# Optimization experiments

Measured on AMD Instinct MI355X. Metric: run time of the kernel, lower is better.

The kernel has to match this reference:

```python
import jax, jax.numpy as jnp
import numpy as np

N = 100000
E = 600000
IN_DIM = 256
H0 = 128
H1 = 64
EPS = 1e-5


def setup_inputs() -> dict:
    key = jax.random.key(0)
    ks = jax.random.split(key, 12)
    x = jax.random.normal(ks[0], (N, IN_DIM), dtype=jnp.float32)
    edge_index = jax.random.randint(ks[1], (2, E), 0, N, dtype=jnp.int64)
    edge_weight = jax.random.uniform(ks[2], (E,), dtype=jnp.float32)
    def lin(k, fan_in, fan_out):
        bound = 1.0 / np.sqrt(fan_in)
        k1, k2 = jax.random.split(k)
        W = jax.random.uniform(k1, (fan_in, fan_out), minval=-bound, maxval=bound, dtype=jnp.float32)
        b = jax.random.uniform(k2, (fan_out,), minval=-bound, maxval=bound, dtype=jnp.float32)
        return W, b
    W0, b0 = lin(ks[3], IN_DIM, H0)
    W1, b1 = lin(ks[4], H0, H0)
    W2, b2 = lin(ks[5], H0, H0)
    pW, pb = lin(ks[6], H0, H1)
    return {
        'x': x, 'edge_index': edge_index, 'edge_weight': edge_weight,
        'bn_gamma': jnp.ones((IN_DIM,), jnp.float32), 'bn_beta': jnp.zeros((IN_DIM,), jnp.float32),
        'W0': W0, 'b0': b0, 'W1': W1, 'b1': b1, 'W2': W2, 'b2': b2,
        'pbn_gamma': jnp.ones((H0,), jnp.float32), 'pbn_beta': jnp.zeros((H0,), jnp.float32),
        'pW': pW, 'pb': pb,
    }


def batchnorm(x, gamma, beta):
    # BatchNorm1d training-mode forward: per-feature batch statistics over nodes
    mean = jnp.mean(x, axis=0)
    var = jnp.mean(jnp.square(x - mean), axis=0)  # biased var, as torch BN forward
    return (x - mean) * jax.lax.rsqrt(var + EPS) * gamma + beta


def gcn_conv(x, src, dst, norm, W, b):
    # PyG GCNConv (add_self_loops=False): transform then normalized aggregation
    h = x @ W                                   # [N, out]
    msg = norm[:, None] * h[src]                # gather + scale, [E, out]
    out = jax.ops.segment_sum(msg, dst, num_segments=N)  # scatter-add
    return out + b


def reference(x, edge_index, edge_weight, bn_gamma, bn_beta, W0, b0, W1, b1, W2, b2, pbn_gamma, pbn_beta, pW, pb):
    src, dst = edge_index[0], edge_index[1]
    # gcn_norm without self loops: D^-1/2 A D^-1/2
    deg = jax.ops.segment_sum(edge_weight, dst, num_segments=N)
    dis = jnp.where(deg > 0, jax.lax.rsqrt(jnp.maximum(deg, EPS)), 0.0)
    norm = dis[src] * edge_weight * dis[dst]    # [E]

    h = batchnorm(x, bn_gamma, bn_beta)
    h = jax.nn.relu(gcn_conv(h, src, dst, norm, W0, b0))
    h = jax.nn.relu(gcn_conv(h, src, dst, norm, W1, b1))
    h = jax.nn.relu(gcn_conv(h, src, dst, norm, W2, b2))
    # project head: BN -> Linear -> ReLU
    h = batchnorm(h, pbn_gamma, pbn_beta)
    h = jax.nn.relu(h @ pW + pb)
    return h
```

## Files before the change

kernel.cpp:

```cpp
#include <hip/hip_runtime.h>


constexpr int NN     = 100000;
constexpr int NEDGE  = 600000;
constexpr int INDIM  = 256;
constexpr int HD     = 128;
constexpr int OUTD   = 64;
#define EPSV 1e-5f

typedef __bf16 bf16x8 __attribute__((ext_vector_type(8)));
typedef float  f32x4  __attribute__((ext_vector_type(4)));

__device__ __forceinline__ float bf2f(unsigned short u) {
    unsigned int v = ((unsigned int)u) << 16;
    return __builtin_bit_cast(float, v);
}
__device__ __forceinline__ unsigned short f2bf(float f) {
    __bf16 h = (__bf16)f;
    return __builtin_bit_cast(unsigned short, h);
}
__device__ __forceinline__ void atomAdd(float* p, float v) {
    unsafeAtomicAdd(p, v);
}

__global__ __launch_bounds__(256) void deghist_k(const int* __restrict__ dst,
                                                 const float* __restrict__ ew,
                                                 float* __restrict__ deg,
                                                 int* __restrict__ cnt, int e) {
    int i = blockIdx.x * blockDim.x + threadIdx.x;
    if (i < e) {
        int d = dst[i];
        atomAdd(&deg[d], ew[i]);
        atomicAdd(&cnt[d], 1);
    }
}

__global__ __launch_bounds__(256) void scan1_k(const int* __restrict__ cnt,
                                               int* __restrict__ rowptr,
                                               int* __restrict__ bsum, int n) {
    __shared__ int s[256];
    int i = blockIdx.x * 256 + threadIdx.x;
    s[threadIdx.x] = (i < n) ? cnt[i] : 0;
    __syncthreads();
    for (int d = 1; d < 256; d <<= 1) {
        int t = (threadIdx.x >= d) ? s[threadIdx.x - d] : 0;
        __syncthreads();
        s[threadIdx.x] += t;
        __syncthreads();
    }
    if (i < n) rowptr[i + 1] = s[threadIdx.x];
    if (threadIdx.x == 255) bsum[blockIdx.x] = s[255];
}

__global__ __launch_bounds__(512) void scan2_k(int* __restrict__ bsum, int nb) {
    __shared__ int s[512];
    s[threadIdx.x] = (threadIdx.x < (unsigned)nb) ? bsum[threadIdx.x] : 0;
    __syncthreads();
    for (int d = 1; d < 512; d <<= 1) {
        int t = (threadIdx.x >= d) ? s[threadIdx.x - d] : 0;
        __syncthreads();
        s[threadIdx.x] += t;
        __syncthreads();
    }
    if (threadIdx.x < (unsigned)nb) bsum[threadIdx.x] = s[threadIdx.x];
}

__global__ __launch_bounds__(256) void scan3_k(int* __restrict__ rowptr,
                                               const int* __restrict__ bsum,
                                               int* __restrict__ cursor, int n) {
    int i = blockIdx.x * 256 + threadIdx.x;
    if (i == 0) { rowptr[0] = 0; cursor[0] = 0; }
    if (i < n) {
        int v = rowptr[i + 1];
        if (blockIdx.x > 0) v += bsum[blockIdx.x - 1];
        rowptr[i + 1] = v;
        if (i + 1 < n) cursor[i + 1] = v;
    }
}

__global__ __launch_bounds__(256) void scatter_k(const int* __restrict__ src,
                                                 const int* __restrict__ dst,
                                                 const float* __restrict__ ew,
                                                 const float* __restrict__ deg,
                                                 int* __restrict__ cursor,
                                                 uint2* __restrict__ edata, int e) {
    int i = blockIdx.x * blockDim.x + threadIdx.x;
    if (i < e) {
        int s = src[i], d = dst[i];
        float ds = deg[s], dd = deg[d];
        float is = ds > 0.f ? rsqrtf(fmaxf(ds, EPSV)) : 0.f;
        float id = dd > 0.f ? rsqrtf(fmaxf(dd, EPSV)) : 0.f;
        float nm = is * ew[i] * id;
        int p = atomicAdd(&cursor[d], 1);
        edata[p] = make_uint2((unsigned)s, __builtin_bit_cast(unsigned, nm));
    }
}

__global__ __launch_bounds__(256) void bn_stats_x_k(const float* __restrict__ in,
                                                    float* __restrict__ sums,
                                                    unsigned short* __restrict__ xb,
                                                    int n) {
    const int tid = threadIdx.x;
    const int cg  = tid & 63;
    const int rs  = tid >> 6;
    float s0 = 0.f, s1 = 0.f, s2 = 0.f, s3 = 0.f;
    float q0 = 0.f, q1 = 0.f, q2 = 0.f, q3 = 0.f;
    for (int r0 = blockIdx.x * 16; r0 < n; r0 += gridDim.x * 16) {
        float4 v[4];
#pragma unroll
        for (int j = 0; j < 4; j++)
            v[j] = *(const float4*)&in[(size_t)(r0 + rs + j * 4) * INDIM + cg * 4];
#pragma unroll
        for (int j = 0; j < 4; j++) {
            s0 += v[j].x; s1 += v[j].y; s2 += v[j].z; s3 += v[j].w;
            q0 += v[j].x * v[j].x; q1 += v[j].y * v[j].y;
            q2 += v[j].z * v[j].z; q3 += v[j].w * v[j].w;
            unsigned int w0 = (unsigned int)f2bf(v[j].x) | ((unsigned int)f2bf(v[j].y) << 16);
            unsigned int w1 = (unsigned int)f2bf(v[j].z) | ((unsigned int)f2bf(v[j].w) << 16);
            *(uint2*)&xb[(size_t)(r0 + rs + j * 4) * INDIM + cg * 4] = make_uint2(w0, w1);
        }
    }
    __shared__ float red[256 * 8];
    red[tid * 8 + 0] = s0; red[tid * 8 + 1] = s1;
    red[tid * 8 + 2] = s2; red[tid * 8 + 3] = s3;
    red[tid * 8 + 4] = q0; red[tid * 8 + 5] = q1;
    red[tid * 8 + 6] = q2; red[tid * 8 + 7] = q3;
    __syncthreads();
    int cgr = tid >> 2, j = tid & 3;
    float a = 0.f, b = 0.f;
#pragma unroll
    for (int r2 = 0; r2 < 4; r2++) {
        a += red[(r2 * 64 + cgr) * 8 + j];
        b += red[(r2 * 64 + cgr) * 8 + 4 + j];
    }
    atomAdd(&sums[tid], a);
    atomAdd(&sums[INDIM + tid], b);
}

__global__ __launch_bounds__(256) void bn_stats16_k(const unsigned short* __restrict__ in,
                                                    float* __restrict__ sums, int n) {
    const int tid = threadIdx.x;
    const int cg  = tid & 15;
    const int rs  = tid >> 4;
    float s[8], q[8];
#pragma unroll
    for (int j = 0; j < 8; j++) { s[j] = 0.f; q[j] = 0.f; }
    for (int r = blockIdx.x * 16 + rs; r < n; r += gridDim.x * 16) {
        uint4 u = *(const uint4*)&in[(size_t)r * HD + cg * 8];
        float v[8];
        v[0] = bf2f((unsigned short)(u.x & 0xffff)); v[1] = bf2f((unsigned short)(u.x >> 16));
        v[2] = bf2f((unsigned short)(u.y & 0xffff)); v[3] = bf2f((unsigned short)(u.y >> 16));
        v[4] = bf2f((unsigned short)(u.z & 0xffff)); v[5] = bf2f((unsigned short)(u.z >> 16));
        v[6] = bf2f((unsigned short)(u.w & 0xffff)); v[7] = bf2f((unsigned short)(u.w >> 16));
#pragma unroll
        for (int j = 0; j < 8; j++) { s[j] += v[j]; q[j] += v[j] * v[j]; }
    }
    __shared__ float red[256 * 16];
#pragma unroll
    for (int j = 0; j < 8; j++) {
        red[tid * 16 + j]     = s[j];
        red[tid * 16 + 8 + j] = q[j];
    }
    __syncthreads();
    if (tid < HD) {
        int cgr = tid >> 3, j = tid & 7;
        float a = 0.f, b = 0.f;
#pragma unroll
        for (int r2 = 0; r2 < 16; r2++) {
            a += red[(r2 * 16 + cgr) * 16 + j];
            b += red[(r2 * 16 + cgr) * 16 + 8 + j];
        }
        atomAdd(&sums[tid], a);
        atomAdd(&sums[HD + tid], b);
    }
}

__global__ __launch_bounds__(256) void wprep1_k(const float* __restrict__ stats,
                                                const float* __restrict__ gamma,
                                                const float* __restrict__ beta,
                                                const float* __restrict__ W0,
                                                const float* __restrict__ W1,
                                                const float* __restrict__ W2,
                                                unsigned short* __restrict__ W0t,
                                                unsigned short* __restrict__ W1t,
                                                unsigned short* __restrict__ W2t,
                                                float* __restrict__ d0, float invN) {
    __shared__ float sA[INDIM], sC[INDIM];
    int f = threadIdx.x;
    {
        float mean = stats[f] * invN;
        float var  = stats[INDIM + f] * invN - mean * mean;
        float a    = gamma[f] * rsqrtf(var + EPSV);
        sA[f] = a;
        sC[f] = beta[f] - mean * a;
    }
    __syncthreads();
    int b = blockIdx.x, tid = threadIdx.x;
    if (b < 128) {
        int i = b * 256 + tid, k = i >> 7, j = i & 127;
        W0t[(size_t)j * INDIM + k] = f2bf(W0[i] * sA[k]);
    } else if (b < 192) {
        int i = (b - 128) * 256 + tid, k = i >> 7, j = i & 127;
        W1t[(size_t)j * HD + k] = f2bf(W1[i]);
    } else if (b < 256) {
        int i = (b - 192) * 256 + tid, k = i >> 7, j = i & 127;
        W2t[(size_t)j * HD + k] = f2bf(W2[i]);
    } else {
        if (tid < HD) {
            float s = 0.f;
            for (int ff = 0; ff < INDIM; ff++) s += sC[ff] * W0[ff * HD + tid];
            d0[tid] = s;
        }
    }
}

__global__ __launch_bounds__(256) void wprep2_k(const float* __restrict__ stats2,
                                                const float* __restrict__ gamma,
                                                const float* __restrict__ beta,
                                                const float* __restrict__ pW,
                                                const float* __restrict__ pb,
                                                unsigned short* __restrict__ pWt,
                                                float* __restrict__ dfin, float invN) {
    __shared__ float sA[HD], sC[HD];
    int f = threadIdx.x;
    if (f < HD) {
        float mean = stats2[f] * invN;
        float var  = stats2[HD + f] * invN - mean * mean;
        float a    = gamma[f] * rsqrtf(var + EPSV);
        sA[f] = a;
        sC[f] = beta[f] - mean * a;
    }
    __syncthreads();
    int b = blockIdx.x, tid = threadIdx.x;
    if (b < 32) {
        int i = b * 256 + tid, k = i >> 6, j = i & 63;
        pWt[(size_t)j * HD + k] = f2bf(pW[i] * sA[k]);
    } else {
        if (tid < OUTD) {
            float s = pb[tid];
            for (int ff = 0; ff < HD; ff++) s += sC[ff] * pW[ff * OUTD + tid];
            dfin[tid] = s;
        }
    }
}

template <int K, int M, bool RELU_OUT, bool OUT_BF16>
__global__ __launch_bounds__(256) void mgemm_k(const unsigned short* __restrict__ A,
                                               const unsigned short* __restrict__ Bt,
                                               const float* __restrict__ outBias,
                                               void* __restrict__ Craw, int n) {
    constexpr int BK  = 64;
    constexpr int LDA = BK + 8;
    __shared__ unsigned short As[128 * LDA];
    __shared__ unsigned short Bs[M * LDA];

    const int tid  = threadIdx.x;
    const int wave = tid >> 6, lane = tid & 63;
    const int quad = lane >> 4, mrow = lane & 15;
    const int row0 = blockIdx.x * 128;

    constexpr int RT = (M == 128) ? 4 : 2;
    constexpr int CT = 4;
    const int rowbase = (M == 128) ? ((wave >> 1) * 64) : (wave * 32);
    const int colbase = (M == 128) ? ((wave & 1) * 64) : 0;

    f32x4 acc[RT][CT];
#pragma unroll
    for (int i = 0; i < RT; i++)
#pragma unroll
        for (int j = 0; j < CT; j++) acc[i][j] = (f32x4){0.f, 0.f, 0.f, 0.f};

    for (int k0 = 0; k0 < K; k0 += BK) {
#pragma unroll
        for (int p = 0; p < 4; p++) {
            int c   = p * 256 + tid;
            int r   = c >> 3;
            int c8  = (c & 7) * 8;
            int grow = row0 + r;
            uint4 u = make_uint4(0, 0, 0, 0);
            if (grow < n) u = *(const uint4*)&A[(size_t)grow * K + k0 + c8];
            *(uint4*)&As[r * LDA + c8] = u;
        }
#pragma unroll
        for (int p = 0; p < M / 32; p++) {
            int c  = p * 256 + tid;
            int r  = c >> 3;
            int c8 = (c & 7) * 8;
            *(uint4*)&Bs[r * LDA + c8] = *(const uint4*)&Bt[(size_t)r * K + k0 + c8];
        }
        __syncthreads();

#pragma unroll
        for (int ks = 0; ks < BK; ks += 32) {
            bf16x8 af[RT], bfr[CT];
#pragma unroll
            for (int i = 0; i < RT; i++)
                af[i] = *(const bf16x8*)&As[(rowbase + i * 16 + mrow) * LDA + ks + quad * 8];
#pragma unroll
            for (int j = 0; j < CT; j++)
                bfr[j] = *(const bf16x8*)&Bs[(colbase + j * 16 + mrow) * LDA + ks + quad * 8];
#pragma unroll
            for (int i = 0; i < RT; i++)
#pragma unroll
                for (int j = 0; j < CT; j++)
                    acc[i][j] = __builtin_amdgcn_mfma_f32_16x16x32_bf16(
                        af[i], bfr[j], acc[i][j], 0, 0, 0);
        }
        __syncthreads();
    }

#pragma unroll
    for (int i = 0; i < RT; i++) {
#pragma unroll
        for (int r = 0; r < 4; r++) {
            int row = row0 + rowbase + i * 16 + quad * 4 + r;
            if (row < n) {
#pragma unroll
                for (int j = 0; j < CT; j++) {
                    int col = colbase + j * 16 + mrow;
                    float v = acc[i][j][r];
                    if (outBias) v += outBias[col];
                    if (RELU_OUT) v = fmaxf(v, 0.f);
                    if (OUT_BF16)
                        ((unsigned short*)Craw)[(size_t)row * M + col] = f2bf(v);
                    else
                        ((float*)Craw)[(size_t)row * M + col] = v;
                }
            }
        }
    }
}

__global__ __launch_bounds__(256) void agg_csr16_k(const unsigned short* __restrict__ t,
                                                   const int* __restrict__ rowptr,
                                                   const uint2* __restrict__ edata,
                                                   const float* __restrict__ bias,
                                                   unsigned short* __restrict__ agg,
                                                   int n) {
    const int tid  = threadIdx.x;
    const int g    = tid >> 4;
    const int gl   = tid & 15;
    const int node = blockIdx.x * 16 + g;
    if (node >= n) return;
    const int beg = rowptr[node], end = rowptr[node + 1];
    float acc[8];
#pragma unroll
    for (int j = 0; j < 8; j++) acc[j] = 0.f;
    const unsigned short* tg = t + gl * 8;
    for (int i = beg; i < end; i += 4) {
        uint4 v[4]; float w[4];
#pragma unroll
        for (int k = 0; k < 4; k++) {
            int  idx = i + k;
            bool ok  = idx < end;
            uint2 ed = edata[ok ? idx : beg];
            w[k] = ok ? __builtin_bit_cast(float, ed.y) : 0.f;
            v[k] = *(const uint4*)&tg[(size_t)ed.x * HD];
        }
#pragma unroll
        for (int k = 0; k < 4; k++) {
            acc[0] += w[k] * bf2f((unsigned short)(v[k].x & 0xffff));
            acc[1] += w[k] * bf2f((unsigned short)(v[k].x >> 16));
            acc[2] += w[k] * bf2f((unsigned short)(v[k].y & 0xffff));
            acc[3] += w[k] * bf2f((unsigned short)(v[k].y >> 16));
            acc[4] += w[k] * bf2f((unsigned short)(v[k].z & 0xffff));
            acc[5] += w[k] * bf2f((unsigned short)(v[k].z >> 16));
            acc[6] += w[k] * bf2f((unsigned short)(v[k].w & 0xffff));
            acc[7] += w[k] * bf2f((unsigned short)(v[k].w >> 16));
        }
    }
    float4 b0 = *(const float4*)&bias[gl * 8];
    float4 b1 = *(const float4*)&bias[gl * 8 + 4];
    float r0 = fmaxf(acc[0] + b0.x, 0.f), r1 = fmaxf(acc[1] + b0.y, 0.f);
    float r2 = fmaxf(acc[2] + b0.z, 0.f), r3 = fmaxf(acc[3] + b0.w, 0.f);
    float r4 = fmaxf(acc[4] + b1.x, 0.f), r5 = fmaxf(acc[5] + b1.y, 0.f);
    float r6 = fmaxf(acc[6] + b1.z, 0.f), r7 = fmaxf(acc[7] + b1.w, 0.f);
    uint4 o;
    o.x = (unsigned int)f2bf(r0) | ((unsigned int)f2bf(r1) << 16);
    o.y = (unsigned int)f2bf(r2) | ((unsigned int)f2bf(r3) << 16);
    o.z = (unsigned int)f2bf(r4) | ((unsigned int)f2bf(r5) << 16);
    o.w = (unsigned int)f2bf(r6) | ((unsigned int)f2bf(r7) << 16);
    *(uint4*)&agg[(size_t)node * HD + gl * 8] = o;
}

extern "C" void kernel_launch(void* const* d_in, const int* in_sizes, int n_in,
                              void* d_out, int out_size, void* d_ws, size_t ws_size,
                              hipStream_t stream) {
    const float* x        = (const float*)d_in[0];
    const int*   ei       = (const int*)d_in[1];
    const float* ew       = (const float*)d_in[2];
    const float* bn_gamma = (const float*)d_in[3];
    const float* bn_beta  = (const float*)d_in[4];
    const float* W0       = (const float*)d_in[5];
    const float* b0       = (const float*)d_in[6];
    const float* W1       = (const float*)d_in[7];
    const float* b1       = (const float*)d_in[8];
    const float* W2       = (const float*)d_in[9];
    const float* b2       = (const float*)d_in[10];
    const float* pgamma   = (const float*)d_in[11];
    const float* pbeta    = (const float*)d_in[12];
    const float* pW       = (const float*)d_in[13];
    const float* pb       = (const float*)d_in[14];
    float* out = (float*)d_out;

    const int* srcp = ei;
    const int* dstp = ei + NEDGE;

    char*  base = (char*)d_ws;
    size_t off  = 0;
    auto carve = [&](size_t bytes) -> void* {
        void* p = (void*)(base + off);
        off = (off + bytes + 255) & ~(size_t)255;
        return p;
    };
    float*          deg    = (float*)carve(NN * 4);
    int*            cnt    = (int*)carve(NN * 4);
    float*          stats  = (float*)carve(2 * INDIM * 4);
    float*          stats2 = (float*)carve(2 * HD * 4);
    int*            rowptr = (int*)carve((NN + 1) * 4);
    int*            cursor = (int*)carve(NN * 4);
    int*            bsum   = (int*)carve(512 * 4);
    uint2*          edata  = (uint2*)carve((size_t)NEDGE * 8);
    float*          d0     = (float*)carve(HD * 4);
    float*          dfin   = (float*)carve(OUTD * 4);
    unsigned short* W0t    = (unsigned short*)carve((size_t)INDIM * HD * 2);
    unsigned short* W1t    = (unsigned short*)carve((size_t)HD * HD * 2);
    unsigned short* W2t    = (unsigned short*)carve((size_t)HD * HD * 2);
    unsigned short* pWt    = (unsigned short*)carve((size_t)HD * OUTD * 2);
    unsigned short* xb     = (unsigned short*)carve((size_t)NN * INDIM * 2);
    unsigned short* tbuf   = (unsigned short*)carve((size_t)NN * HD * 2);
    unsigned short* aggb   = (unsigned short*)carve((size_t)NN * HD * 2);
    (void)ws_size;

    const int eBlocks  = (NEDGE + 255) / 256;
    const int nBlocks  = (NN + 255) / 256;
    const int gemmGrid = (NN + 127) / 128;
    const int aggGrid  = (NN + 15) / 16;

    hipMemsetAsync(deg, 0, (size_t)((char*)cnt - (char*)deg) + NN * 4, stream);
    hipMemsetAsync(stats, 0, (size_t)((char*)stats2 - (char*)stats) + 2 * HD * 4, stream);

    deghist_k<<<eBlocks, 256, 0, stream>>>(dstp, ew, deg, cnt, NEDGE);
    scan1_k<<<nBlocks, 256, 0, stream>>>(cnt, rowptr, bsum, NN);
    scan2_k<<<1, 512, 0, stream>>>(bsum, nBlocks);
    scan3_k<<<nBlocks, 256, 0, stream>>>(rowptr, bsum, cursor, NN);
    scatter_k<<<eBlocks, 256, 0, stream>>>(srcp, dstp, ew, deg, cursor, edata, NEDGE);

    bn_stats_x_k<<<1024, 256, 0, stream>>>(x, stats, xb, NN);
    wprep1_k<<<257, 256, 0, stream>>>(stats, bn_gamma, bn_beta, W0, W1, W2,
                                      W0t, W1t, W2t, d0, 1.f / NN);

    mgemm_k<INDIM, HD, false, true><<<gemmGrid, 256, 0, stream>>>(
        xb, W0t, d0, tbuf, NN);
    agg_csr16_k<<<aggGrid, 256, 0, stream>>>(tbuf, rowptr, edata, b0, aggb, NN);

    mgemm_k<HD, HD, false, true><<<gemmGrid, 256, 0, stream>>>(
        aggb, W1t, nullptr, tbuf, NN);
    agg_csr16_k<<<aggGrid, 256, 0, stream>>>(tbuf, rowptr, edata, b1, aggb, NN);

    mgemm_k<HD, HD, false, true><<<gemmGrid, 256, 0, stream>>>(
        aggb, W2t, nullptr, tbuf, NN);
    agg_csr16_k<<<aggGrid, 256, 0, stream>>>(tbuf, rowptr, edata, b2, aggb, NN);

    bn_stats16_k<<<512, 256, 0, stream>>>(aggb, stats2, NN);
    wprep2_k<<<33, 256, 0, stream>>>(stats2, pgamma, pbeta, pW, pb, pWt, dfin,
                                     1.f / NN);
    mgemm_k<HD, OUTD, true, false><<<gemmGrid, 256, 0, stream>>>(
        aggb, pWt, dfin, out, NN);

    (void)n_in; (void)in_sizes; (void)out_size;
}
```

Before: 484.2 us.

## Fuse GCN aggregation with next-layer GEMM and merge independent setup kernels

Merges independent preprocessing kernels into combined launches split by block index: degree histogram with BN stats, scan with weight prep, and edge scatter with the first GEMM. It also fuses each CSR aggregation with the following layer's MFMA GEMM through shared memory, and fuses the last aggregation with the BN statistics pass. The goal is to cut kernel launch count and avoid writing and re-reading the intermediate aggregated activations in global memory. In exchange, the fused aggregate+GEMM kernel runs only one 128-row block per tile with heavy shared memory use, which may lower occupancy for the latency-bound gather phase.

New measurement: 474.2 us. 1.02x faster.

```diff
diff --git a/kernel.cpp b/kernel.cpp
--- a/kernel.cpp
+++ b/kernel.cpp
@@ -1,11 +1,17 @@
 #include <hip/hip_runtime.h>
 
 
-constexpr int NN     = 100000;
-constexpr int NEDGE  = 600000;
-constexpr int INDIM  = 256;
-constexpr int HD     = 128;
-constexpr int OUTD   = 64;
+constexpr int NN    = 100000;
+constexpr int NEDGE = 600000;
+constexpr int INDIM = 256;
+constexpr int HD    = 128;
+constexpr int OUTD  = 64;
+constexpr int EB    = (NEDGE + 255) / 256;
+constexpr int SB    = 1024;
+constexpr int NB    = (NN + 255) / 256;
+constexpr int WB    = 257;
+constexpr int GG    = (NN + 127) / 128;
+constexpr int A2B   = 1024;
 #define EPSV 1e-5f
 
 typedef __bf16 bf16x8 __attribute__((ext_vector_type(8)));
@@ -23,93 +29,245 @@
     unsafeAtomicAdd(p, v);
 }
 
-__global__ __launch_bounds__(256) void deghist_k(const int* __restrict__ dst,
-                                                 const float* __restrict__ ew,
-                                                 float* __restrict__ deg,
-                                                 int* __restrict__ cnt, int e) {
-    int i = blockIdx.x * blockDim.x + threadIdx.x;
-    if (i < e) {
-        int d = dst[i];
-        atomAdd(&deg[d], ew[i]);
-        atomicAdd(&cnt[d], 1);
-    }
-}
-
-__global__ __launch_bounds__(256) void scan1_k(const int* __restrict__ cnt,
-                                               int* __restrict__ rowptr,
-                                               int* __restrict__ bsum, int n) {
-    __shared__ int s[256];
-    int i = blockIdx.x * 256 + threadIdx.x;
-    s[threadIdx.x] = (i < n) ? cnt[i] : 0;
-    __syncthreads();
-    for (int d = 1; d < 256; d <<= 1) {
-        int t = (threadIdx.x >= d) ? s[threadIdx.x - d] : 0;
+template <int K, int M, bool RELU_OUT, bool OUT_BF16>
+__device__ __forceinline__ void mgemm_body(int bid, int tid, char* smem,
+                                           const unsigned short* __restrict__ A,
+                                           const unsigned short* __restrict__ Bt,
+                                           const float* __restrict__ outBias,
+                                           void* __restrict__ Craw, int n) {
+    constexpr int BK  = 64;
+    constexpr int LDA = BK + 8;
+    unsigned short* As = (unsigned short*)smem;
+    unsigned short* Bs = As + 128 * LDA;
+
+    const int wave = tid >> 6, lane = tid & 63;
+    const int quad = lane >> 4, mrow = lane & 15;
+    const int row0 = bid * 128;
+
+    constexpr int RT = (M == 128) ? 4 : 2;
+    constexpr int CT = 4;
+    const int rowbase = (M == 128) ? ((wave >> 1) * 64) : (wave * 32);
+    const int colbase = (M == 128) ? ((wave & 1) * 64) : 0;
+
+    f32x4 acc[RT][CT];
+#pragma unroll
+    for (int i = 0; i < RT; i++)
+#pragma unroll
+        for (int j = 0; j < CT; j++) acc[i][j] = (f32x4){0.f, 0.f, 0.f, 0.f};
+
+    for (int k0 = 0; k0 < K; k0 += BK) {
+        if (k0) __syncthreads();
+#pragma unroll
+        for (int p = 0; p < 4; p++) {
+            int c   = p * 256 + tid;
+            int r   = c >> 3;
+            int c8  = (c & 7) * 8;
+            int grow = row0 + r;
+            uint4 u = make_uint4(0, 0, 0, 0);
+            if (grow < n) u = *(const uint4*)&A[(size_t)grow * K + k0 + c8];
+            *(uint4*)&As[r * LDA + c8] = u;
+        }
+#pragma unroll
+        for (int p = 0; p < M / 32; p++) {
+            int c  = p * 256 + tid;
+            int r  = c >> 3;
+            int c8 = (c & 7) * 8;
+            *(uint4*)&Bs[r * LDA + c8] = *(const uint4*)&Bt[(size_t)r * K + k0 + c8];
+        }
         __syncthreads();
-        s[threadIdx.x] += t;
+
+#pragma unroll
+        for (int ks = 0; ks < BK; ks += 32) {
+            bf16x8 af[RT], bfr[CT];
+#pragma unroll
+            for (int i = 0; i < RT; i++)
+                af[i] = *(const bf16x8*)&As[(rowbase + i * 16 + mrow) * LDA + ks + quad * 8];
+#pragma unroll
+            for (int j = 0; j < CT; j++)
+                bfr[j] = *(const bf16x8*)&Bs[(colbase + j * 16 + mrow) * LDA + ks + quad * 8];
+#pragma unroll
+            for (int i = 0; i < RT; i++)
+#pragma unroll
+                for (int j = 0; j < CT; j++)
+                    acc[i][j] = __builtin_amdgcn_mfma_f32_16x16x32_bf16(
+                        af[i], bfr[j], acc[i][j], 0, 0, 0);
+        }
+    }
+
+#pragma unroll
+    for (int i = 0; i < RT; i++) {
+#pragma unroll
+        for (int r = 0; r < 4; r++) {
+            int row = row0 + rowbase + i * 16 + quad * 4 + r;
+            if (row < n) {
+#pragma unroll
+                for (int j = 0; j < CT; j++) {
+                    int col = colbase + j * 16 + mrow;
+                    float v = acc[i][j][r];
+                    if (outBias) v += outBias[col];
+                    if (RELU_OUT) v = fmaxf(v, 0.f);
+                    if (OUT_BF16)
+                        ((unsigned short*)Craw)[(size_t)row * M + col] = f2bf(v);
+                    else
+                        ((float*)Craw)[(size_t)row * M + col] = v;
+                }
+            }
+        }
+    }
+}
+
+__device__ __forceinline__ void gather8(const unsigned short* __restrict__ tg,
+                                        const uint2* __restrict__ edata,
+                                        int i, int beg, int end, float* acc) {
+    uint4 v[8]; float w[8];
+#pragma unroll
+    for (int k = 0; k < 8; k++) {
+        int  idx = i + k;
+        bool ok  = idx < end;
+        uint2 ed = edata[ok ? idx : beg];
+        w[k] = ok ? __builtin_bit_cast(float, ed.y) : 0.f;
+        v[k] = *(const uint4*)&tg[(size_t)ed.x * HD];
+    }
+#pragma unroll
+    for (int k = 0; k < 8; k++) {
+        acc[0] += w[k] * bf2f((unsigned short)(v[k].x & 0xffff));
+        acc[1] += w[k] * bf2f((unsigned short)(v[k].x >> 16));
+        acc[2] += w[k] * bf2f((unsigned short)(v[k].y & 0xffff));
+        acc[3] += w[k] * bf2f((unsigned short)(v[k].y >> 16));
+        acc[4] += w[k] * bf2f((unsigned short)(v[k].z & 0xffff));
+        acc[5] += w[k] * bf2f((unsigned short)(v[k].z >> 16));
+        acc[6] += w[k] * bf2f((unsigned short)(v[k].w & 0xffff));
+        acc[7] += w[k] * bf2f((unsigned short)(v[k].w >> 16));
+    }
+}
+
+__global__ __launch_bounds__(256) void fagg_gemm_k(const unsigned short* __restrict__ t,
+                                                   const int* __restrict__ rowptr,
+                                                   const uint2* __restrict__ edata,
+                                                   const float* __restrict__ bias,
+                                                   const unsigned short* __restrict__ Bt,
+                                                   unsigned short* __restrict__ Cout,
+                                                   int n) {
+    constexpr int LDAa = HD + 8;
+    constexpr int LDAb = 64 + 8;
+    __shared__ unsigned short As[128 * LDAa];
+    __shared__ unsigned short Bs[HD * LDAb];
+
+    const int tid  = threadIdx.x;
+    const int row0 = blockIdx.x * 128;
+
+    {
+        const int g  = tid >> 4;
+        const int gl = tid & 15;
+        const unsigned short* tg = t + gl * 8;
+        float4 bb0 = *(const float4*)&bias[gl * 8];
+        float4 bb1 = *(const float4*)&bias[gl * 8 + 4];
+        for (int rr = 0; rr < 8; rr++) {
+            int node = row0 + g * 8 + rr;
+            float acc[8];
+#pragma unroll
+            for (int j = 0; j < 8; j++) acc[j] = 0.f;
+            if (node < n) {
+                int beg = rowptr[node], end = rowptr[node + 1];
+                for (int i = beg; i < end; i += 8)
+                    gather8(tg, edata, i, beg, end, acc);
+            }
+            float r0 = fmaxf(acc[0] + bb0.x, 0.f), r1 = fmaxf(acc[1] + bb0.y, 0.f);
+            float r2 = fmaxf(acc[2] + bb0.z, 0.f), r3 = fmaxf(acc[3] + bb0.w, 0.f);
+            float r4 = fmaxf(acc[4] + bb1.x, 0.f), r5 = fmaxf(acc[5] + bb1.y, 0.f);
+            float r6 = fmaxf(acc[6] + bb1.z, 0.f), r7 = fmaxf(acc[7] + bb1.w, 0.f);
+            uint4 o;
+            o.x = (unsigned int)f2bf(r0) | ((unsigned int)f2bf(r1) << 16);
+            o.y = (unsigned int)f2bf(r2) | ((unsigned int)f2bf(r3) << 16);
+            o.z = (unsigned int)f2bf(r4) | ((unsigned int)f2bf(r5) << 16);
+            o.w = (unsigned int)f2bf(r6) | ((unsigned int)f2bf(r7) << 16);
+            *(uint4*)&As[(g * 8 + rr) * LDAa + gl * 8] = o;
+        }
+    }
+
+    const int wave = tid >> 6, lane = tid & 63;
+    const int quad = lane >> 4, mrow = lane & 15;
+    const int rowbase = (wave >> 1) * 64;
+    const int colbase = (wave & 1) * 64;
+
+    f32x4 acc[4][4];
+#pragma unroll
+    for (int i = 0; i < 4; i++)
+#pragma unroll
+        for (int j = 0; j < 4; j++) acc[i][j] = (f32x4){0.f, 0.f, 0.f, 0.f};
+
+    for (int k0 = 0; k0 < HD; k0 += 64) {
+        if (k0) __syncthreads();
+#pragma unroll
+        for (int p = 0; p < 4; p++) {
+            int c  = p * 256 + tid;
+            int r  = c >> 3;
+            int c8 = (c & 7) * 8;
+            *(uint4*)&Bs[r * LDAb + c8] = *(const uint4*)&Bt[(size_t)r * HD + k0 + c8];
+        }
         __syncthreads();
-    }
-    if (i < n) rowptr[i + 1] = s[threadIdx.x];
-    if (threadIdx.x == 255) bsum[blockIdx.x] = s[255];
-}
-
-__global__ __launch_bounds__(512) void scan2_k(int* __restrict__ bsum, int nb) {
-    __shared__ int s[512];
-    s[threadIdx.x] = (threadIdx.x < (unsigned)nb) ? bsum[threadIdx.x] : 0;
-    __syncthreads();
-    for (int d = 1; d < 512; d <<= 1) {
-        int t = (threadIdx.x >= d) ? s[threadIdx.x - d] : 0;
-        __syncthreads();
-        s[threadIdx.x] += t;
-        __syncthreads();
-    }
-    if (threadIdx.x < (unsigned)nb) bsum[threadIdx.x] = s[threadIdx.x];
-}
-
-__global__ __launch_bounds__(256) void scan3_k(int* __restrict__ rowptr,
-                                               const int* __restrict__ bsum,
-                                               int* __restrict__ cursor, int n) {
-    int i = blockIdx.x * 256 + threadIdx.x;
-    if (i == 0) { rowptr[0] = 0; cursor[0] = 0; }
-    if (i < n) {
-        int v = rowptr[i + 1];
-        if (blockIdx.x > 0) v += bsum[blockIdx.x - 1];
-        rowptr[i + 1] = v;
-        if (i + 1 < n) cursor[i + 1] = v;
-    }
-}
-
-__global__ __launch_bounds__(256) void scatter_k(const int* __restrict__ src,
-                                                 const int* __restrict__ dst,
-                                                 const float* __restrict__ ew,
-                                                 const float* __restrict__ deg,
-                                                 int* __restrict__ cursor,
-                                                 uint2* __restrict__ edata, int e) {
-    int i = blockIdx.x * blockDim.x + threadIdx.x;
-    if (i < e) {
-        int s = src[i], d = dst[i];
-        float ds = deg[s], dd = deg[d];
-        float is = ds > 0.f ? rsqrtf(fmaxf(ds, EPSV)) : 0.f;
-        float id = dd > 0.f ? rsqrtf(fmaxf(dd, EPSV)) : 0.f;
-        float nm = is * ew[i] * id;
-        int p = atomicAdd(&cursor[d], 1);
-        edata[p] = make_uint2((unsigned)s, __builtin_bit_cast(unsigned, nm));
-    }
-}
-
-__global__ __launch_bounds__(256) void bn_stats_x_k(const float* __restrict__ in,
-                                                    float* __restrict__ sums,
-                                                    unsigned short* __restrict__ xb,
-                                                    int n) {
+#pragma unroll
+        for (int ks = 0; ks < 64; ks += 32) {
+            bf16x8 af[4], bfr[4];
+#pragma unroll
+            for (int i = 0; i < 4; i++)
+                af[i] = *(const bf16x8*)&As[(rowbase + i * 16 + mrow) * LDAa + k0 + ks + quad * 8];
+#pragma unroll
+            for (int j = 0; j < 4; j++)
+                bfr[j] = *(const bf16x8*)&Bs[(colbase + j * 16 + mrow) * LDAb + ks + quad * 8];
+#pragma unroll
+            for (int i = 0; i < 4; i++)
+#pragma unroll
+                for (int j = 0; j < 4; j++)
+                    acc[i][j] = __builtin_amdgcn_mfma_f32_16x16x32_bf16(
+                        af[i], bfr[j], acc[i][j], 0, 0, 0);
+        }
+    }
+
+#pragma unroll
+    for (int i = 0; i < 4; i++) {
+#pragma unroll
+        for (int r = 0; r < 4; r++) {
+            int row = row0 + rowbase + i * 16 + quad * 4 + r;
+            if (row < n) {
+#pragma unroll
+                for (int j = 0; j < 4; j++) {
+                    int col = colbase + j * 16 + mrow;
+                    Cout[(size_t)row * HD + col] = f2bf(acc[i][j][r]);
+                }
+            }
+        }
+    }
+}
+
+__global__ __launch_bounds__(256) void front_k(const int* __restrict__ dst,
+                                               const float* __restrict__ ew,
+                                               float* __restrict__ deg,
+                                               int* __restrict__ cnt,
+                                               const float* __restrict__ x,
+                                               float* __restrict__ sums,
+                                               unsigned short* __restrict__ xb) {
+    __shared__ float red[256 * 8];
     const int tid = threadIdx.x;
+    if (blockIdx.x < EB) {
+        int i = blockIdx.x * 256 + tid;
+        if (i < NEDGE) {
+            int d = dst[i];
+            atomAdd(&deg[d], ew[i]);
+            atomicAdd(&cnt[d], 1);
+        }
+        return;
+    }
+    const int bid = blockIdx.x - EB;
     const int cg  = tid & 63;
     const int rs  = tid >> 6;
     float s0 = 0.f, s1 = 0.f, s2 = 0.f, s3 = 0.f;
     float q0 = 0.f, q1 = 0.f, q2 = 0.f, q3 = 0.f;
-    for (int r0 = blockIdx.x * 16; r0 < n; r0 += gridDim.x * 16) {
+    for (int r0 = bid * 16; r0 < NN; r0 += SB * 16) {
         float4 v[4];
 #pragma unroll
         for (int j = 0; j < 4; j++)
-            v[j] = *(const float4*)&in[(size_t)(r0 + rs + j * 4) * INDIM + cg * 4];
+            v[j] = *(const float4*)&x[(size_t)(r0 + rs + j * 4) * INDIM + cg * 4];
 #pragma unroll
         for (int j = 0; j < 4; j++) {
             s0 += v[j].x; s1 += v[j].y; s2 += v[j].z; s3 += v[j].w;
@@ -120,7 +278,6 @@
             *(uint2*)&xb[(size_t)(r0 + rs + j * 4) * INDIM + cg * 4] = make_uint2(w0, w1);
         }
     }
-    __shared__ float red[256 * 8];
     red[tid * 8 + 0] = s0; red[tid * 8 + 1] = s1;
     red[tid * 8 + 2] = s2; red[tid * 8 + 3] = s3;
     red[tid * 8 + 4] = q0; red[tid * 8 + 5] = q1;
@@ -137,65 +294,47 @@
     atomAdd(&sums[INDIM + tid], b);
 }
 
-__global__ __launch_bounds__(256) void bn_stats16_k(const unsigned short* __restrict__ in,
-                                                    float* __restrict__ sums, int n) {
+__global__ __launch_bounds__(256) void mid_k(const int* __restrict__ cnt,
+                                             int* __restrict__ rowptr,
+                                             int* __restrict__ bsum,
+                                             const float* __restrict__ stats,
+                                             const float* __restrict__ gamma,
+                                             const float* __restrict__ beta,
+                                             const float* __restrict__ W0,
+                                             const float* __restrict__ W1,
+                                             const float* __restrict__ W2,
+                                             unsigned short* __restrict__ W0t,
+                                             unsigned short* __restrict__ W1t,
+                                             unsigned short* __restrict__ W2t,
+                                             float* __restrict__ d0, float invN) {
+    __shared__ float sm[512];
     const int tid = threadIdx.x;
-    const int cg  = tid & 15;
-    const int rs  = tid >> 4;
-    float s[8], q[8];
-#pragma unroll
-    for (int j = 0; j < 8; j++) { s[j] = 0.f; q[j] = 0.f; }
-    for (int r = blockIdx.x * 16 + rs; r < n; r += gridDim.x * 16) {
-        uint4 u = *(const uint4*)&in[(size_t)r * HD + cg * 8];
-        float v[8];
-        v[0] = bf2f((unsigned short)(u.x & 0xffff)); v[1] = bf2f((unsigned short)(u.x >> 16));
-        v[2] = bf2f((unsigned short)(u.y & 0xffff)); v[3] = bf2f((unsigned short)(u.y >> 16));
-        v[4] = bf2f((unsigned short)(u.z & 0xffff)); v[5] = bf2f((unsigned short)(u.z >> 16));
-        v[6] = bf2f((unsigned short)(u.w & 0xffff)); v[7] = bf2f((unsigned short)(u.w >> 16));
-#pragma unroll
-        for (int j = 0; j < 8; j++) { s[j] += v[j]; q[j] += v[j] * v[j]; }
-    }
-    __shared__ float red[256 * 16];
-#pragma unroll
-    for (int j = 0; j < 8; j++) {
-        red[tid * 16 + j]     = s[j];
-        red[tid * 16 + 8 + j] = q[j];
+    if (blockIdx.x < NB) {
+        int* s = (int*)sm;
+        int i = blockIdx.x * 256 + tid;
+        s[tid] = (i < NN) ? cnt[i] : 0;
+        __syncthreads();
+        for (int d = 1; d < 256; d <<= 1) {
+            int t = (tid >= d) ? s[tid - d] : 0;
+            __syncthreads();
+            s[tid] += t;
+            __syncthreads();
+        }
+        if (i < NN) rowptr[i + 1] = s[tid];
+        if (tid == 255) bsum[blockIdx.x] = s[255];
+        return;
+    }
+    const int b = blockIdx.x - NB;
+    float* sA = sm;
+    float* sC = sm + 256;
+    {
+        float mean = stats[tid] * invN;
+        float var  = stats[INDIM + tid] * invN - mean * mean;
+        float a    = gamma[tid] * rsqrtf(var + EPSV);
+        sA[tid] = a;
+        sC[tid] = beta[tid] - mean * a;
     }
     __syncthreads();
-    if (tid < HD) {
-        int cgr = tid >> 3, j = tid & 7;
-        float a = 0.f, b = 0.f;
-#pragma unroll
-        for (int r2 = 0; r2 < 16; r2++) {
-            a += red[(r2 * 16 + cgr) * 16 + j];
-            b += red[(r2 * 16 + cgr) * 16 + 8 + j];
-        }
-        atomAdd(&sums[tid], a);
-        atomAdd(&sums[HD + tid], b);
-    }
-}
-
-__global__ __launch_bounds__(256) void wprep1_k(const float* __restrict__ stats,
-                                                const float* __restrict__ gamma,
-                                                const float* __restrict__ beta,
-                                                const float* __restrict__ W0,
-                                                const float* __restrict__ W1,
-                                                const float* __restrict__ W2,
-                                                unsigned short* __restrict__ W0t,
-                                                unsigned short* __restrict__ W1t,
-                                                unsigned short* __restrict__ W2t,
-                                                float* __restrict__ d0, float invN) {
-    __shared__ float sA[INDIM], sC[INDIM];
-    int f = threadIdx.x;
-    {
-        float mean = stats[f] * invN;
-        float var  = stats[INDIM + f] * invN - mean * mean;
-        float a    = gamma[f] * rsqrtf(var + EPSV);
-        sA[f] = a;
-        sC[f] = beta[f] - mean * a;
-    }
-    __syncthreads();
-    int b = blockIdx.x, tid = threadIdx.x;
     if (b < 128) {
         int i = b * 256 + tid, k = i >> 7, j = i & 127;
         W0t[(size_t)j * INDIM + k] = f2bf(W0[i] * sA[k]);
@@ -211,6 +350,121 @@
             for (int ff = 0; ff < INDIM; ff++) s += sC[ff] * W0[ff * HD + tid];
             d0[tid] = s;
         }
+    }
+}
+
+__global__ __launch_bounds__(512) void scan2_k(int* __restrict__ bsum, int nb) {
+    __shared__ int s[512];
+    s[threadIdx.x] = (threadIdx.x < (unsigned)nb) ? bsum[threadIdx.x] : 0;
+    __syncthreads();
+    for (int d = 1; d < 512; d <<= 1) {
+        int t = (threadIdx.x >= d) ? s[threadIdx.x - d] : 0;
+        __syncthreads();
+        s[threadIdx.x] += t;
+        __syncthreads();
+    }
+    if (threadIdx.x < (unsigned)nb) bsum[threadIdx.x] = s[threadIdx.x];
+}
+
+__global__ __launch_bounds__(256) void scan3_k(int* __restrict__ rowptr,
+                                               const int* __restrict__ bsum,
+                                               int* __restrict__ cursor, int n) {
+    int i = blockIdx.x * 256 + threadIdx.x;
+    if (i == 0) { rowptr[0] = 0; cursor[0] = 0; }
+    if (i < n) {
+        int v = rowptr[i + 1];
+        if (blockIdx.x > 0) v += bsum[blockIdx.x - 1];
+        rowptr[i + 1] = v;
+        if (i + 1 < n) cursor[i + 1] = v;
+    }
+}
+
+__global__ __launch_bounds__(256) void sg0_k(const int* __restrict__ src,
+                                             const int* __restrict__ dst,
+                                             const float* __restrict__ ew,
+                                             const float* __restrict__ deg,
+                                             int* __restrict__ cursor,
+                                             uint2* __restrict__ edata,
+                                             const unsigned short* __restrict__ xb,
+                                             const unsigned short* __restrict__ W0t,
+                                             const float* __restrict__ d0,
+                                             unsigned short* __restrict__ tbufA) {
+    __shared__ char smem[(128 * 72 + 128 * 72) * 2];
+    if (blockIdx.x < EB) {
+        int i = blockIdx.x * 256 + threadIdx.x;
+        if (i < NEDGE) {
+            int s = src[i], d = dst[i];
+            float ds = deg[s], dd = deg[d];
+            float is = ds > 0.f ? rsqrtf(fmaxf(ds, EPSV)) : 0.f;
+            float id = dd > 0.f ? rsqrtf(fmaxf(dd, EPSV)) : 0.f;
+            float nm = is * ew[i] * id;
+            int p = atomicAdd(&cursor[d], 1);
+            edata[p] = make_uint2((unsigned)s, __builtin_bit_cast(unsigned, nm));
+        }
+        return;
+    }
+    mgemm_body<INDIM, HD, false, true>(blockIdx.x - EB, threadIdx.x, smem,
+                                       xb, W0t, d0, tbufA, NN);
+}
+
+__global__ __launch_bounds__(256) void agg2_stats_k(const unsigned short* __restrict__ t,
+                                                    const int* __restrict__ rowptr,
+                                                    const uint2* __restrict__ edata,
+                                                    const float* __restrict__ bias,
+                                                    unsigned short* __restrict__ agg,
+                                                    float* __restrict__ sums, int n) {
+    const int tid = threadIdx.x, g = tid >> 4, gl = tid & 15;
+    const unsigned short* tg = t + gl * 8;
+    float4 bb0 = *(const float4*)&bias[gl * 8];
+    float4 bb1 = *(const float4*)&bias[gl * 8 + 4];
+    float ssum[8], ssq[8];
+#pragma unroll
+    for (int j = 0; j < 8; j++) { ssum[j] = 0.f; ssq[j] = 0.f; }
+
+    for (int node0 = blockIdx.x * 16; node0 < n; node0 += A2B * 16) {
+        int node = node0 + g;
+        float acc[8];
+#pragma unroll
+        for (int j = 0; j < 8; j++) acc[j] = 0.f;
+        if (node < n) {
+            int beg = rowptr[node], end = rowptr[node + 1];
+            for (int i = beg; i < end; i += 8)
+                gather8(tg, edata, i, beg, end, acc);
+        }
+        float r[8];
+        r[0] = fmaxf(acc[0] + bb0.x, 0.f); r[1] = fmaxf(acc[1] + bb0.y, 0.f);
+        r[2] = fmaxf(acc[2] + bb0.z, 0.f); r[3] = fmaxf(acc[3] + bb0.w, 0.f);
+        r[4] = fmaxf(acc[4] + bb1.x, 0.f); r[5] = fmaxf(acc[5] + bb1.y, 0.f);
+        r[6] = fmaxf(acc[6] + bb1.z, 0.f); r[7] = fmaxf(acc[7] + bb1.w, 0.f);
+        if (node < n) {
+            uint4 o;
+            o.x = (unsigned int)f2bf(r[0]) | ((unsigned int)f2bf(r[1]) << 16);
+            o.y = (unsigned int)f2bf(r[2]) | ((unsigned int)f2bf(r[3]) << 16);
+            o.z = (unsigned int)f2bf(r[4]) | ((unsigned int)f2bf(r[5]) << 16);
+            o.w = (unsigned int)f2bf(r[6]) | ((unsigned int)f2bf(r[7]) << 16);
+            *(uint4*)&agg[(size_t)node * HD + gl * 8] = o;
+#pragma unroll
+            for (int j = 0; j < 8; j++) { ssum[j] += r[j]; ssq[j] += r[j] * r[j]; }
+        }
+    }
+
+    __shared__ float red[256 * 16];
+#pragma unroll
+    for (int j = 0; j < 8; j++) {
+        red[tid * 16 + j]     = ssum[j];
+        red[tid * 16 + 8 + j] = ssq[j];
+    }
+    __syncthreads();
+    if (tid < HD) {
+        int glr = tid >> 3, j = tid & 7;
+        float a = 0.f, b = 0.f;
+#pragma unroll
+        for (int g2 = 0; g2 < 16; g2++) {
+            a += red[(g2 * 16 + glr) * 16 + j];
+            b += red[(g2 * 16 + glr) * 16 + 8 + j];
+        }
+        atomAdd(&sums[tid], a);
+        atomAdd(&sums[HD + tid], b);
     }
 }
 
@@ -244,143 +498,13 @@
     }
 }
 
-template <int K, int M, bool RELU_OUT, bool OUT_BF16>
-__global__ __launch_bounds__(256) void mgemm_k(const unsigned short* __restrict__ A,
+__global__ __launch_bounds__(256) void gemm3_k(const unsigned short* __restrict__ A,
                                                const unsigned short* __restrict__ Bt,
                                                const float* __restrict__ outBias,
-                                               void* __restrict__ Craw, int n) {
-    constexpr int BK  = 64;
-    constexpr int LDA = BK + 8;
-    __shared__ unsigned short As[128 * LDA];
-    __shared__ unsigned short Bs[M * LDA];
-
-    const int tid  = threadIdx.x;
-    const int wave = tid >> 6, lane = tid & 63;
-    const int quad = lane >> 4, mrow = lane & 15;
-    const int row0 = blockIdx.x * 128;
-
-    constexpr int RT = (M == 128) ? 4 : 2;
-    constexpr int CT = 4;
-    const int rowbase = (M == 128) ? ((wave >> 1) * 64) : (wave * 32);
-    const int colbase = (M == 128) ? ((wave & 1) * 64) : 0;
-
-    f32x4 acc[RT][CT];
-#pragma unroll
-    for (int i = 0; i < RT; i++)
-#pragma unroll
-        for (int j = 0; j < CT; j++) acc[i][j] = (f32x4){0.f, 0.f, 0.f, 0.f};
-
-    for (int k0 = 0; k0 < K; k0 += BK) {
-#pragma unroll
-        for (int p = 0; p < 4; p++) {
-            int c   = p * 256 + tid;
-            int r   = c >> 3;
-            int c8  = (c & 7) * 8;
-            int grow = row0 + r;
-            uint4 u = make_uint4(0, 0, 0, 0);
-            if (grow < n) u = *(const uint4*)&A[(size_t)grow * K + k0 + c8];
-            *(uint4*)&As[r * LDA + c8] = u;
-        }
-#pragma unroll
-        for (int p = 0; p < M / 32; p++) {
-            int c  = p * 256 + tid;
-            int r  = c >> 3;
-            int c8 = (c & 7) * 8;
-            *(uint4*)&Bs[r * LDA + c8] = *(const uint4*)&Bt[(size_t)r * K + k0 + c8];
-        }
-        __syncthreads();
-
-#pragma unroll
-        for (int ks = 0; ks < BK; ks += 32) {
-            bf16x8 af[RT], bfr[CT];
-#pragma unroll
-            for (int i = 0; i < RT; i++)
-                af[i] = *(const bf16x8*)&As[(rowbase + i * 16 + mrow) * LDA + ks + quad * 8];
-#pragma unroll
-            for (int j = 0; j < CT; j++)
-                bfr[j] = *(const bf16x8*)&Bs[(colbase + j * 16 + mrow) * LDA + ks + quad * 8];
-#pragma unroll
-            for (int i = 0; i < RT; i++)
-#pragma unroll
-                for (int j = 0; j < CT; j++)
-                    acc[i][j] = __builtin_amdgcn_mfma_f32_16x16x32_bf16(
-                        af[i], bfr[j], acc[i][j], 0, 0, 0);
-        }
-        __syncthreads();
-    }
-
-#pragma unroll
-    for (int i = 0; i < RT; i++) {
-#pragma unroll
-        for (int r = 0; r < 4; r++) {
-            int row = row0 + rowbase + i * 16 + quad * 4 + r;
-            if (row < n) {
-#pragma unroll
-                for (int j = 0; j < CT; j++) {
-                    int col = colbase + j * 16 + mrow;
-                    float v = acc[i][j][r];
-                    if (outBias) v += outBias[col];
-                    if (RELU_OUT) v = fmaxf(v, 0.f);
-                    if (OUT_BF16)
-                        ((unsigned short*)Craw)[(size_t)row * M + col] = f2bf(v);
-                    else
-                        ((float*)Craw)[(size_t)row * M + col] = v;
-                }
-            }
-        }
-    }
-}
-
-__global__ __launch_bounds__(256) void agg_csr16_k(const unsigned short* __restrict__ t,
-                                                   const int* __restrict__ rowptr,
-                                                   const uint2* __restrict__ edata,
-                                                   const float* __restrict__ bias,
-                                                   unsigned short* __restrict__ agg,
-                                                   int n) {
-    const int tid  = threadIdx.x;
-    const int g    = tid >> 4;
-    const int gl   = tid & 15;
-    const int node = blockIdx.x * 16 + g;
-    if (node >= n) return;
-    const int beg = rowptr[node], end = rowptr[node + 1];
-    float acc[8];
-#pragma unroll
-    for (int j = 0; j < 8; j++) acc[j] = 0.f;
-    const unsigned short* tg = t + gl * 8;
-    for (int i = beg; i < end; i += 4) {
-        uint4 v[4]; float w[4];
-#pragma unroll
-        for (int k = 0; k < 4; k++) {
-            int  idx = i + k;
-            bool ok  = idx < end;
-            uint2 ed = edata[ok ? idx : beg];
-            w[k] = ok ? __builtin_bit_cast(float, ed.y) : 0.f;
-            v[k] = *(const uint4*)&tg[(size_t)ed.x * HD];
-        }
-#pragma unroll
-        for (int k = 0; k < 4; k++) {
-            acc[0] += w[k] * bf2f((unsigned short)(v[k].x & 0xffff));
-            acc[1] += w[k] * bf2f((unsigned short)(v[k].x >> 16));
-            acc[2] += w[k] * bf2f((unsigned short)(v[k].y & 0xffff));
-            acc[3] += w[k] * bf2f((unsigned short)(v[k].y >> 16));
-            acc[4] += w[k] * bf2f((unsigned short)(v[k].z & 0xffff));
-            acc[5] += w[k] * bf2f((unsigned short)(v[k].z >> 16));
-            acc[6] += w[k] * bf2f((unsigned short)(v[k].w & 0xffff));
-            acc[7] += w[k] * bf2f((unsigned short)(v[k].w >> 16));
-        }
-    }
-    float4 b0 = *(const float4*)&bias[gl * 8];
-    float4 b1 = *(const float4*)&bias[gl * 8 + 4];
-    float r0 = fmaxf(acc[0] + b0.x, 0.f), r1 = fmaxf(acc[1] + b0.y, 0.f);
-    float r2 = fmaxf(acc[2] + b0.z, 0.f), r3 = fmaxf(acc[3] + b0.w, 0.f);
-    float r4 = fmaxf(acc[4] + b1.x, 0.f), r5 = fmaxf(acc[5] + b1.y, 0.f);
-    float r6 = fmaxf(acc[6] + b1.z, 0.f), r7 = fmaxf(acc[7] + b1.w, 0.f);
-    uint4 o;
-    o.x = (unsigned int)f2bf(r0) | ((unsigned int)f2bf(r1) << 16);
-    o.y = (unsigned int)f2bf(r2) | ((unsigned int)f2bf(r3) << 16);
-    o.z = (unsigned int)f2bf(r4) | ((unsigned int)f2bf(r5) << 16);
-    o.w = (unsigned int)f2bf(r6) | ((unsigned int)f2bf(r7) << 16);
-    *(uint4*)&agg[(size_t)node * HD + gl * 8] = o;
+                                               float* __restrict__ C, int n) {
+    __shared__ char smem[(128 * 72 + OUTD * 72) * 2];
+    mgemm_body<HD, OUTD, true, false>(blockIdx.x, threadIdx.x, smem,
+                                      A, Bt, outBias, C, n);
 }
 
 extern "C" void kernel_launch(void* const* d_in, const int* in_sizes, int n_in,
@@ -428,45 +552,31 @@
     unsigned short* W2t    = (unsigned short*)carve((size_t)HD * HD * 2);
     unsigned short* pWt    = (unsigned short*)carve((size_t)HD * OUTD * 2);
     unsigned short* xb     = (unsigned short*)carve((size_t)NN * INDIM * 2);
-    unsigned short* tbuf   = (unsigned short*)carve((size_t)NN * HD * 2);
+    unsigned short* tbufA  = (unsigned short*)carve((size_t)NN * HD * 2);
+    unsigned short* tbufB  = (unsigned short*)carve((size_t)NN * HD * 2);
     unsigned short* aggb   = (unsigned short*)carve((size_t)NN * HD * 2);
     (void)ws_size;
 
-    const int eBlocks  = (NEDGE + 255) / 256;
-    const int nBlocks  = (NN + 255) / 256;
-    const int gemmGrid = (NN + 127) / 128;
-    const int aggGrid  = (NN + 15) / 16;
-
-    hipMemsetAsync(deg, 0, (size_t)((char*)cnt - (char*)deg) + NN * 4, stream);
-    hipMemsetAsync(stats, 0, (size_t)((char*)stats2 - (char*)stats) + 2 * HD * 4, stream);
-
-    deghist_k<<<eBlocks, 256, 0, stream>>>(dstp, ew, deg, cnt, NEDGE);
-    scan1_k<<<nBlocks, 256, 0, stream>>>(cnt, rowptr, bsum, NN);
-    scan2_k<<<1, 512, 0, stream>>>(bsum, nBlocks);
-    scan3_k<<<nBlocks, 256, 0, stream>>>(rowptr, bsum, cursor, NN);
-    scatter_k<<<eBlocks, 256, 0, stream>>>(srcp, dstp, ew, deg, cursor, edata, NEDGE);
-
-    bn_stats_x_k<<<1024, 256, 0, stream>>>(x, stats, xb, NN);
-    wprep1_k<<<257, 256, 0, stream>>>(stats, bn_gamma, bn_beta, W0, W1, W2,
-                                      W0t, W1t, W2t, d0, 1.f / NN);
-
-    mgemm_k<INDIM, HD, false, true><<<gemmGrid, 256, 0, stream>>>(
-        xb, W0t, d0, tbuf, NN);
-    agg_csr16_k<<<aggGrid, 256, 0, stream>>>(tbuf, rowptr, edata, b0, aggb, NN);
-
-    mgemm_k<HD, HD, false, true><<<gemmGrid, 256, 0, stream>>>(
-        aggb, W1t, nullptr, tbuf, NN);
-    agg_csr16_k<<<aggGrid, 256, 0, stream>>>(tbuf, rowptr, edata, b1, aggb, NN);
-
-    mgemm_k<HD, HD, false, true><<<gemmGrid, 256, 0, stream>>>(
-        aggb, W2t, nullptr, tbuf, NN);
-    agg_csr16_k<<<aggGrid, 256, 0, stream>>>(tbuf, rowptr, edata, b2, aggb, NN);
-
-    bn_stats16_k<<<512, 256, 0, stream>>>(aggb, stats2, NN);
+    hipMemsetAsync(deg, 0, (size_t)((char*)stats2 - (char*)deg) + 2 * HD * 4, stream);
+
+    front_k<<<EB + SB, 256, 0, stream>>>(dstp, ew, deg, cnt, x, stats, xb);
+
+    mid_k<<<NB + WB, 256, 0, stream>>>(cnt, rowptr, bsum, stats, bn_gamma, bn_beta,
+                                       W0, W1, W2, W0t, W1t, W2t, d0, 1.f / NN);
+    scan2_k<<<1, 512, 0, stream>>>(bsum, NB);
+    scan3_k<<<NB, 256, 0, stream>>>(rowptr, bsum, cursor, NN);
+
+    sg0_k<<<EB + GG, 256, 0, stream>>>(srcp, dstp, ew, deg, cursor, edata,
+                                       xb, W0t, d0, tbufA);
+
+    fagg_gemm_k<<<GG, 256, 0, stream>>>(tbufA, rowptr, edata, b0, W1t, tbufB, NN);
+    fagg_gemm_k<<<GG, 256, 0, stream>>>(tbufB, rowptr, edata, b1, W2t, tbufA, NN);
+
+    agg2_stats_k<<<A2B, 256, 0, stream>>>(tbufA, rowptr, edata, b2, aggb, stats2, NN);
+
     wprep2_k<<<33, 256, 0, stream>>>(stats2, pgamma, pbeta, pW, pb, pWt, dfin,
                                      1.f / NN);
-    mgemm_k<HD, OUTD, true, false><<<gemmGrid, 256, 0, stream>>>(
-        aggb, pWt, dfin, out, NN);
+    gemm3_k<<<GG, 256, 0, stream>>>(aggb, pWt, dfin, out, NN);
 
     (void)n_in; (void)in_sizes; (void)out_size;
 }
```
